# Optimization experiments

Measured on AMD Instinct MI355X. Metric: run time of the kernel, lower is better.

## Reference

```python
import jax, jax.numpy as jnp
import numpy as np

B, S, D = 8, 1024, 768
H, DQK, DV = 12, 64, 64
DHEAD = 2 * DQK + DV  # 192, interleaved per-head qkv layout
DOUT = 768


def setup_inputs() -> dict:
    key = jax.random.key(0)
    k1, k2, k3, k4 = jax.random.split(key, 4)
    x = jax.random.normal(k1, (B, S, D), dtype=jnp.float32)
    w_qkv = jax.random.normal(k2, (D, H * DHEAD), dtype=jnp.float32) * (D ** -0.5)
    w_out = jax.random.normal(k3, (H * DV, DOUT), dtype=jnp.float32) * ((H * DV) ** -0.5)
    b_out = jax.random.normal(k4, (DOUT,), dtype=jnp.float32) * 0.02
    return {"x": x, "w_qkv": w_qkv, "w_out": w_out, "b_out": b_out}


def reference(x, w_qkv, w_out, b_out):
    scale = DQK ** -0.5
    # Interleaved per-head layout: [B,S,H,DHEAD] then split into q|k|v blocks.
    qkv = (x @ w_qkv).reshape(B, S, H, DHEAD)
    q = qkv[..., :DQK]                 # [B,S,H,DQK]
    k = qkv[..., DQK:2 * DQK]          # [B,S,H,DQK]
    v = qkv[..., 2 * DQK:]             # [B,S,H,DV]
    scores = jnp.einsum("bshd,bthd->bhst", q, k) * scale  # [B,H,S,S]
    attn = jax.nn.softmax(scores, axis=-1)
    out = jnp.einsum("bhst,bthd->bshd", attn, v)           # [B,S,H,DV]
    out = out.reshape(B, S, H * DV)
    return out @ w_out + b_out
```

## Files before the change

### kernel.cpp

```cpp
#include <hip/hip_runtime.h>
#include <hip/hip_bf16.h>
#include <cstdint>

namespace {

constexpr int kB = 8;
constexpr int kS = 1024;
constexpr int kD = 768;
constexpr int kH = 12;
constexpr int kDH = 192;
constexpr int kNQ = kH * kDH;
constexpr int kNK = kH * 128;
constexpr int kM = kB * kS;
constexpr int kDO = 768;

using f32x4 = __attribute__((ext_vector_type(4))) float;
using s16x8 = __attribute__((ext_vector_type(8))) short;
using u16x8 = __attribute__((ext_vector_type(8))) unsigned short;
using u16x4 = __attribute__((ext_vector_type(4))) unsigned short;

__device__ __forceinline__ unsigned short f2bf(float f) {
  union { float f; uint32_t u; } v; v.f = f;
  uint32_t u = v.u;
  u += 0x7FFFu + ((u >> 16) & 1u);
  return (unsigned short)(u >> 16);
}

__device__ __forceinline__ void load_lds16(const void* g, void* l) {
  __builtin_amdgcn_global_load_lds((__attribute__((address_space(1))) void*)g,
                                   (__attribute__((address_space(3))) void*)l,
                                   16, 0, 0);
}


__global__ __launch_bounds__(256) void cvt_x_kernel(const float* __restrict__ in,
                                                    unsigned short* __restrict__ out) {
  int i = (blockIdx.x * 256 + threadIdx.x) * 8;
  float4 a = *(const float4*)(in + i);
  float4 b = *(const float4*)(in + i + 4);
  u16x8 o;
  o[0] = f2bf(a.x); o[1] = f2bf(a.y); o[2] = f2bf(a.z); o[3] = f2bf(a.w);
  o[4] = f2bf(b.x); o[5] = f2bf(b.y); o[6] = f2bf(b.z); o[7] = f2bf(b.w);
  *(u16x8*)(out + i) = o;
}

__global__ __launch_bounds__(256) void cvt_transpose_kernel(const float* __restrict__ w,
                                                            unsigned short* __restrict__ wt,
                                                            int K, int N) {
  __shared__ float tile[32][33];
  int k0 = blockIdx.x * 32, n0 = blockIdx.y * 32;
  int tx = threadIdx.x & 31, ty = threadIdx.x >> 5;
  #pragma unroll
  for (int r = 0; r < 32; r += 8)
    tile[ty + r][tx] = w[(size_t)(k0 + ty + r) * N + n0 + tx];
  __syncthreads();
  #pragma unroll
  for (int r = 0; r < 32; r += 8)
    wt[(size_t)(n0 + ty + r) * K + k0 + tx] = f2bf(tile[tx][ty + r]);
}

template <int MODE>
__global__ __launch_bounds__(256, 2) void gemm_bt_kernel(
    const unsigned short* __restrict__ A,
    const unsigned short* __restrict__ Bt,
    void* __restrict__ Cout,
    unsigned short* __restrict__ Vtg,
    const float* __restrict__ bias,
    int M, int N, int K) {
  __shared__ alignas(16) unsigned short Al[128 * 64];
  __shared__ alignas(16) unsigned short Bl[128 * 64];
  const int nT = N >> 7;
  const int tm = blockIdx.x / nT, tn = blockIdx.x % nT;
  const int tid = threadIdx.x;
  const int w = tid >> 6, l = tid & 63;
  const int wr = w >> 1, wc = w & 1;
  const int la = l & 15, g = l >> 4;
  const int sr = l >> 3, sc = l & 7;

  f32x4 acc[4][4] = {};
  const unsigned short* Ag = A + (size_t)(tm * 128) * K;
  const unsigned short* Bg = Bt + (size_t)(tn * 128) * K;

  for (int k0 = 0; k0 < K; k0 += 64) {
    #pragma unroll
    for (int j = 0; j < 4; ++j) {
      int row = w * 32 + j * 8 + sr;
      load_lds16(Ag + (size_t)row * K + k0 + sc * 8, &Al[row * 64 + sc * 8]);
      load_lds16(Bg + (size_t)row * K + k0 + sc * 8, &Bl[row * 64 + sc * 8]);
    }
    __syncthreads();
    #pragma unroll
    for (int kk = 0; kk < 2; ++kk) {
      s16x8 af[4], bfv[4];
      #pragma unroll
      for (int i = 0; i < 4; ++i)
        af[i] = *(const s16x8*)&Al[(wr * 64 + i * 16 + la) * 64 + kk * 32 + g * 8];
      #pragma unroll
      for (int j = 0; j < 4; ++j)
        bfv[j] = *(const s16x8*)&Bl[(wc * 64 + j * 16 + la) * 64 + kk * 32 + g * 8];
      #pragma unroll
      for (int i = 0; i < 4; ++i)
        #pragma unroll
        for (int j = 0; j < 4; ++j)
          acc[i][j] = __builtin_amdgcn_mfma_f32_16x16x32_bf16(af[i], bfv[j], acc[i][j], 0, 0, 0);
    }
    __syncthreads();
  }

  #pragma unroll
  for (int i = 0; i < 4; ++i) {
    int row0 = tm * 128 + wr * 64 + i * 16 + g * 4;
    #pragma unroll
    for (int j = 0; j < 4; ++j) {
      int col = tn * 128 + wc * 64 + j * 16 + la;
      if (MODE == 0) {
        int h = col / kDH, colm = col % kDH;
        if (colm < 128) {
          unsigned short* C = (unsigned short*)Cout;
          float sc2 = (colm < 64) ? 0.125f : 1.0f;
          int ncol = h * 128 + colm;
          #pragma unroll
          for (int r = 0; r < 4; ++r)
            C[(size_t)(row0 + r) * kNK + ncol] = f2bf(acc[i][j][r] * sc2);
        } else {
          int d = colm - 128;
          int bb = row0 >> 10, t = row0 & 1023;
          u16x4 pv;
          #pragma unroll
          for (int r = 0; r < 4; ++r) pv[r] = f2bf(acc[i][j][r]);
          *(u16x4*)&Vtg[((size_t)(bb * kH + h) * 64 + d) * kS + t] = pv;
        }
      } else {
        float* C = (float*)Cout;
        float bv = bias[col];
        #pragma unroll
        for (int r = 0; r < 4; ++r)
          C[(size_t)(row0 + r) * N + col] = acc[i][j][r] + bv;
      }
    }
  }
}

__global__ __launch_bounds__(256, 8) void attn_kernel(
    const unsigned short* __restrict__ qk,
    const unsigned short* __restrict__ Vtg,
    unsigned short* __restrict__ Ab) {
  const int qb = blockIdx.x, h = blockIdx.y, b = blockIdx.z;
  const int tid = threadIdx.x;
  const int w = tid >> 6, l = tid & 63;
  const int la = l & 15, g = l >> 4;

  __shared__ alignas(16) unsigned short Kl[64 * 64];
  __shared__ alignas(16) unsigned short Vl[64 * 64];
  __shared__ alignas(16) unsigned short Pl[64 * 64];

  const size_t base_bs = (size_t)b * kS;
  const size_t qrow0 = base_bs + (size_t)qb * 64;

  s16x8 qf[2];
  {
    const unsigned short* qp = qk + (qrow0 + w * 16 + la) * kNK + h * 128;
    qf[0] = *(const s16x8*)(qp + g * 8);
    qf[1] = *(const s16x8*)(qp + 32 + g * 8);
  }

  const int c0 = w * 64 + l;
  const int c1 = 256 + w * 64 + l;
  const int r0 = c0 >> 3, cc0 = (c0 & 7) ^ (r0 & 7);
  const int r1 = c1 >> 3, cc1 = (c1 & 7) ^ (r1 & 7);
  const unsigned short* Kg = qk + (base_bs)*kNK + h * 128 + 64;
  const unsigned short* Vg = Vtg + (size_t)(b * kH + h) * 64 * kS;

  float mrow[4], lrow[4];
  #pragma unroll
  for (int r = 0; r < 4; ++r) { mrow[r] = -1e30f; lrow[r] = 0.f; }
  f32x4 oacc[4] = {};
  const float LOG2E = 1.44269504088896340736f;

  for (int kt = 0; kt < 16; ++kt) {
    __syncthreads();
    load_lds16(Kg + (size_t)(kt * 64 + r0) * kNK + cc0 * 8, &Kl[c0 * 8]);
    load_lds16(Kg + (size_t)(kt * 64 + r1) * kNK + cc1 * 8, &Kl[c1 * 8]);
    load_lds16(Vg + (size_t)r0 * kS + kt * 64 + cc0 * 8, &Vl[c0 * 8]);
    load_lds16(Vg + (size_t)r1 * kS + kt * 64 + cc1 * 8, &Vl[c1 * 8]);
    __syncthreads();

    f32x4 sacc[4] = {};
    #pragma unroll
    for (int ks = 0; ks < 2; ++ks) {
      #pragma unroll
      for (int tb = 0; tb < 4; ++tb) {
        int row = tb * 16 + la;
        s16x8 kf = *(const s16x8*)&Kl[row * 64 + (((ks * 4 + g) ^ (row & 7)) * 8)];
        sacc[tb] = __builtin_amdgcn_mfma_f32_16x16x32_bf16(qf[ks], kf, sacc[tb], 0, 0, 0);
      }
    }

    #pragma unroll
    for (int r = 0; r < 4; ++r) {
      float m = fmaxf(fmaxf(sacc[0][r], sacc[1][r]), fmaxf(sacc[2][r], sacc[3][r]));
      #pragma unroll
      for (int msk = 1; msk < 16; msk <<= 1) m = fmaxf(m, __shfl_xor(m, msk, 64));
      float mnew = fmaxf(mrow[r], m);
      float corr = exp2f((mrow[r] - mnew) * LOG2E);
      mrow[r] = mnew;
      float s = 0.f;
      #pragma unroll
      for (int tb = 0; tb < 4; ++tb) {
        float p = exp2f((sacc[tb][r] - mnew) * LOG2E);
        sacc[tb][r] = p;
        s += p;
      }
      #pragma unroll
      for (int msk = 1; msk < 16; msk <<= 1) s += __shfl_xor(s, msk, 64);
      lrow[r] = lrow[r] * corr + s;
      #pragma unroll
      for (int db = 0; db < 4; ++db) oacc[db][r] *= corr;
    }

    #pragma unroll
    for (int r = 0; r < 4; ++r) {
      int prow = w * 16 + g * 4 + r, x = prow & 7;
      #pragma unroll
      for (int tb = 0; tb < 4; ++tb) {
        int col = tb * 16 + la;
        Pl[prow * 64 + (col ^ (x << 3))] = f2bf(sacc[tb][r]);
      }
    }

    #pragma unroll
    for (int ks = 0; ks < 2; ++ks) {
      int prow = w * 16 + la;
      s16x8 pf = *(const s16x8*)&Pl[prow * 64 + (((ks * 4 + g) ^ (prow & 7)) * 8)];
      #pragma unroll
      for (int db = 0; db < 4; ++db) {
        int drow = db * 16 + la;
        s16x8 vf = *(const s16x8*)&Vl[drow * 64 + (((ks * 4 + g) ^ (drow & 7)) * 8)];
        oacc[db] = __builtin_amdgcn_mfma_f32_16x16x32_bf16(pf, vf, oacc[db], 0, 0, 0);
      }
    }
  }

  #pragma unroll
  for (int db = 0; db < 4; ++db) {
    #pragma unroll
    for (int r = 0; r < 4; ++r) {
      int row = w * 16 + g * 4 + r;
      Ab[(qrow0 + row) * (size_t)(kH * 64) + h * 64 + db * 16 + la] =
          f2bf(oacc[db][r] / lrow[r]);
    }
  }
}

}

extern "C" void kernel_launch(void* const* d_in, const int* in_sizes, int n_in,
                              void* d_out, int out_size, void* d_ws, size_t ws_size,
                              hipStream_t stream) {
  (void)in_sizes; (void)n_in; (void)out_size; (void)ws_size;
  const float* x = (const float*)d_in[0];
  const float* w_qkv = (const float*)d_in[1];
  const float* w_out = (const float*)d_in[2];
  const float* b_out = (const float*)d_in[3];

  unsigned short* Xb = (unsigned short*)d_ws;
  unsigned short* WqT = Xb + (size_t)kM * kD;
  unsigned short* WoT = WqT + (size_t)kNQ * kD;
  unsigned short* QK = WoT + (size_t)kDO * kDO;
  unsigned short* Vtg = QK + (size_t)kM * kNK;
  unsigned short* Ab = Vtg + (size_t)kB * kH * 64 * kS;

  cvt_x_kernel<<<dim3((kM * kD) / (256 * 8)), dim3(256), 0, stream>>>(x, Xb);
  cvt_transpose_kernel<<<dim3(kD / 32, kNQ / 32), dim3(256), 0, stream>>>(w_qkv, WqT, kD, kNQ);
  cvt_transpose_kernel<<<dim3(kDO / 32, kDO / 32), dim3(256), 0, stream>>>(w_out, WoT, kDO, kDO);

  gemm_bt_kernel<0><<<dim3((kM / 128) * (kNQ / 128)), dim3(256), 0, stream>>>(
      Xb, WqT, (void*)QK, Vtg, nullptr, kM, kNQ, kD);

  attn_kernel<<<dim3(kS / 64, kH, kB), dim3(256), 0, stream>>>(QK, Vtg, Ab);

  gemm_bt_kernel<1><<<dim3((kM / 128) * (kDO / 128)), dim3(256), 0, stream>>>(
      Ab, WoT, d_out, nullptr, b_out, kM, kDO, kH * 64);
}
```

Before: 252.5 us.

## Rewrite attention with 32x32 MFMA, register-resident P and lazy rescaling

```diff
diff --git a/kernel.cpp b/kernel.cpp
--- a/kernel.cpp
+++ b/kernel.cpp
@@ -15,6 +15,7 @@
 constexpr int kDO = 768;
 
 using f32x4 = __attribute__((ext_vector_type(4))) float;
+using f32x16 = __attribute__((ext_vector_type(16))) float;
 using s16x8 = __attribute__((ext_vector_type(8))) short;
 using u16x8 = __attribute__((ext_vector_type(8))) unsigned short;
 using u16x4 = __attribute__((ext_vector_type(4))) unsigned short;
@@ -26,10 +27,32 @@
   return (unsigned short)(u >> 16);
 }
 
+__device__ __forceinline__ unsigned packbf(float a, float b) {
+  return (unsigned)f2bf(a) | ((unsigned)f2bf(b) << 16);
+}
+
 __device__ __forceinline__ void load_lds16(const void* g, void* l) {
   __builtin_amdgcn_global_load_lds((__attribute__((address_space(1))) void*)g,
                                    (__attribute__((address_space(3))) void*)l,
                                    16, 0, 0);
+}
+
+__device__ __forceinline__ s16x8 repack8(int hi, float p0, float p1, float p2, float p3,
+                                         float p4, float p5, float p6, float p7) {
+  unsigned x0 = packbf(p0, p1);
+  unsigned x1 = packbf(p2, p3);
+  unsigned x2 = packbf(p4, p5);
+  unsigned x3 = packbf(p6, p7);
+  unsigned y0 = (unsigned)__shfl_xor((int)x0, 32, 64);
+  unsigned y1 = (unsigned)__shfl_xor((int)x1, 32, 64);
+  unsigned y2 = (unsigned)__shfl_xor((int)x2, 32, 64);
+  unsigned y3 = (unsigned)__shfl_xor((int)x3, 32, 64);
+  union { unsigned u[4]; s16x8 v; } r;
+  r.u[0] = hi ? y2 : x0;
+  r.u[1] = hi ? y3 : x1;
+  r.u[2] = hi ? x2 : y0;
+  r.u[3] = hi ? x3 : y1;
+  return r.v;
 }
 
 
@@ -121,7 +144,9 @@
           int ncol = h * 128 + colm;
           #pragma unroll
           for (int r = 0; r < 4; ++r)
-            C[(size_t)(row0 + r) * kNK + ncol] = f2bf(acc[i][j][r] * sc2);
+            C[(size_t)(row0 + r) * kNK + ncol] = f2bf(acc[i][j][r]
+
+ * sc2);
         } else {
           int d = colm - 128;
           int bb = row0 >> 10, t = row0 & 1023;
@@ -141,41 +166,43 @@
   }
 }
 
-__global__ __launch_bounds__(256, 8) void attn_kernel(
+__global__ __launch_bounds__(256, 3) void attn_kernel(
     const unsigned short* __restrict__ qk,
     const unsigned short* __restrict__ Vtg,
     unsigned short* __restrict__ Ab) {
-  const int qb = blockIdx.x, h = blockIdx.y, b = blockIdx.z;
+  const int id = blockIdx.x;
+  const int b = id & 7;
+  const int h = (id >> 3) % kH;
+  const int qb = id / (kH * 8);
   const int tid = threadIdx.x;
   const int w = tid >> 6, l = tid & 63;
-  const int la = l & 15, g = l >> 4;
+  const int q0 = l & 31, hi = l >> 5;
 
   __shared__ alignas(16) unsigned short Kl[64 * 64];
   __shared__ alignas(16) unsigned short Vl[64 * 64];
-  __shared__ alignas(16) unsigned short Pl[64 * 64];
 
   const size_t base_bs = (size_t)b * kS;
-  const size_t qrow0 = base_bs + (size_t)qb * 64;
-
-  s16x8 qf[2];
+  const size_t qrow0 = base_bs + (size_t)qb * 128;
+  const size_t myq = qrow0 + w * 32 + q0;
+
+  s16x8 qf[4];
   {
-    const unsigned short* qp = qk + (qrow0 + w * 16 + la) * kNK + h * 128;
-    qf[0] = *(const s16x8*)(qp + g * 8);
-    qf[1] = *(const s16x8*)(qp + 32 + g * 8);
+    const unsigned short* qp = qk + myq * kNK + h * 128 + hi * 8;
+    #pragma unroll
+    for (int kg = 0; kg < 4; ++kg) qf[kg] = *(const s16x8*)(qp + kg * 16);
   }
 
   const int c0 = w * 64 + l;
   const int c1 = 256 + w * 64 + l;
   const int r0 = c0 >> 3, cc0 = (c0 & 7) ^ (r0 & 7);
   const int r1 = c1 >> 3, cc1 = (c1 & 7) ^ (r1 & 7);
-  const unsigned short* Kg = qk + (base_bs)*kNK + h * 128 + 64;
+  const unsigned short* Kg = qk + base_bs * kNK + h * 128 + 64;
   const unsigned short* Vg = Vtg + (size_t)(b * kH + h) * 64 * kS;
 
-  float mrow[4], lrow[4];
-  #pragma unroll
-  for (int r = 0; r < 4; ++r) { mrow[r] = -1e30f; lrow[r] = 0.f; }
-  f32x4 oacc[4] = {};
   const float LOG2E = 1.44269504088896340736f;
+  float m2 = -1e30f;
+  float lrow = 0.f;
+  f32x16 oacc[2] = {};
 
   for (int kt = 0; kt < 16; ++kt) {
     __syncthreads();
@@ -185,71 +212,83 @@
     load_lds16(Vg + (size_t)r1 * kS + kt * 64 + cc1 * 8, &Vl[c1 * 8]);
     __syncthreads();
 
-    f32x4 sacc[4] = {};
-    #pragma unroll
-    for (int ks = 0; ks < 2; ++ks) {
-      #pragma unroll
-      for (int tb = 0; tb < 4; ++tb) {
-        int row = tb * 16 + la;
-        s16x8 kf = *(const s16x8*)&Kl[row * 64 + (((ks * 4 + g) ^ (row & 7)) * 8)];
-        sacc[tb] = __builtin_amdgcn_mfma_f32_16x16x32_bf16(qf[ks], kf, sacc[tb], 0, 0, 0);
+    f32x16 sacc[2] = {};
+    #pragma unroll
+    for (int tb = 0; tb < 2; ++tb) {
+      const int tl = tb * 32 + q0, xr = tl & 7;
+      #pragma unroll
+      for (int kg = 0; kg < 4; ++kg) {
+        s16x8 kf = *(const s16x8*)&Kl[tl * 64 + (((kg * 2 + hi) ^ xr) * 8)];
+        sacc[tb] = __builtin_amdgcn_mfma_f32_32x32x16_bf16(kf, qf[kg], sacc[tb], 0, 0, 0);
       }
     }
 
-    #pragma unroll
-    for (int r = 0; r < 4; ++r) {
-      float m = fmaxf(fmaxf(sacc[0][r], sacc[1][r]), fmaxf(sacc[2][r], sacc[3][r]));
-      #pragma unroll
-      for (int msk = 1; msk < 16; msk <<= 1) m = fmaxf(m, __shfl_xor(m, msk, 64));
-      float mnew = fmaxf(mrow[r], m);
-      float corr = exp2f((mrow[r] - mnew) * LOG2E);
-      mrow[r] = mnew;
-      float s = 0.f;
-      #pragma unroll
-      for (int tb = 0; tb < 4; ++tb) {
-        float p = exp2f((sacc[tb][r] - mnew) * LOG2E);
-        sacc[tb][r] = p;
-        s += p;
-      }
-      #pragma unroll
-      for (int msk = 1; msk < 16; msk <<= 1) s += __shfl_xor(s, msk, 64);
-      lrow[r] = lrow[r] * corr + s;
-      #pragma unroll
-      for (int db = 0; db < 4; ++db) oacc[db][r] *= corr;
-    }
-
-    #pragma unroll
-    for (int r = 0; r < 4; ++r) {
-      int prow = w * 16 + g * 4 + r, x = prow & 7;
-      #pragma unroll
-      for (int tb = 0; tb < 4; ++tb) {
-        int col = tb * 16 + la;
-        Pl[prow * 64 + (col ^ (x << 3))] = f2bf(sacc[tb][r]);
-      }
-    }
-
-    #pragma unroll
-    for (int ks = 0; ks < 2; ++ks) {
-      int prow = w * 16 + la;
-      s16x8 pf = *(const s16x8*)&Pl[prow * 64 + (((ks * 4 + g) ^ (prow & 7)) * 8)];
-      #pragma unroll
-      for (int db = 0; db < 4; ++db) {
-        int drow = db * 16 + la;
-        s16x8 vf = *(const s16x8*)&Vl[drow * 64 + (((ks * 4 + g) ^ (drow & 7)) * 8)];
-        oacc[db] = __builtin_amdgcn_mfma_f32_16x16x32_bf16(pf, vf, oacc[db], 0, 0, 0);
-      }
+    float mx[16];
+    #pragma unroll
+    for (int r = 0; r < 16; ++r) mx[r] = fmaxf(sacc[0][r], sacc[1][r]);
+    #pragma unroll
+    for (int s2 = 8; s2 >= 1; s2 >>= 1)
+      #pragma unroll
+      for (int r = 0; r < s2; ++r) mx[r] = fmaxf(mx[r], mx[r + s2]);
+    float pmax = fmaxf(mx[0], __shfl_xor(mx[0], 32, 64));
+    float rx2 = pmax * LOG2E;
+    if (!__all(rx2 - m2 <= 11.5416f)) {
+      float m2n = fmaxf(m2, rx2);
+      float corr = exp2f(m2 - m2n);
+      m2 = m2n;
+      lrow *= corr;
+      #pragma unroll
+      for (int db = 0; db < 2; ++db)
+        #pragma unroll
+        for (int r = 0; r < 16; ++r) oacc[db][r] *= corr;
+    }
+
+    float p[32];
+    #pragma unroll
+    for (int tb = 0; tb < 2; ++tb)
+      #pragma unroll
+      for (int r = 0; r < 16; ++r)
+        p[tb * 16 + r] = exp2f(fmaf(sacc[tb][r], LOG2E, -m2));
+
+    float sm[16];
+    #pragma unroll
+    for (int r = 0; r < 16; ++r) sm[r] = p[r] + p[16 + r];
+    #pragma unroll
+    for (int s2 = 8; s2 >= 1; s2 >>= 1)
+      #pragma unroll
+      for (int r = 0; r < s2; ++r) sm[r] += sm[r + s2];
+    lrow += sm[0] + __shfl_xor(sm[0], 32, 64);
+
+    s16x8 pb0 = repack8(hi, p[0], p[1], p[2], p[3], p[4], p[5], p[6], p[7]);
+    s16x8 pb1 = repack8(hi, p[8], p[9], p[10], p[11], p[12], p[13], p[14], p[15]);
+    s16x8 pb2 = repack8(hi, p[16], p[17], p[18], p[19], p[20], p[21], p[22], p[23]);
+    s16x8 pb3 = repack8(hi, p[24], p[25], p[26], p[27], p[28], p[29], p[30], p[31]);
+
+    #pragma unroll
+    for (int db = 0; db < 2; ++db) {
+      const int dl = db * 32 + q0, xr = dl & 7;
+      s16x8 v0 = *(const s16x8*)&Vl[dl * 64 + (((0 + hi) ^ xr) * 8)];
+      s16x8 v1 = *(const s16x8*)&Vl[dl * 64 + (((2 + hi) ^ xr) * 8)];
+      s16x8 v2 = *(const s16x8*)&Vl[dl * 64 + (((4 + hi) ^ xr) * 8)];
+      s16x8 v3 = *(const s16x8*)&Vl[dl * 64 + (((6 + hi) ^ xr) * 8)];
+      oacc[db] = __builtin_amdgcn_mfma_f32_32x32x16_bf16(v0, pb0, oacc[db], 0, 0, 0);
+      oacc[db] = __builtin_amdgcn_mfma_f32_32x32x16_bf16(v1, pb1, oacc[db], 0, 0, 0);
+      oacc[db] = __builtin_amdgcn_mfma_f32_32x32x16_bf16(v2, pb2, oacc[db], 0, 0, 0);
+      oacc[db] = __builtin_amdgcn_mfma_f32_32x32x16_bf16(v3, pb3, oacc[db], 0, 0, 0);
     }
   }
 
+  float inv = 1.0f / lrow;
+  unsigned short* dst = Ab + myq * (size_t)(kH * 64) + h * 64;
   #pragma unroll
-  for (int db = 0; db < 4; ++db) {
-    #pragma unroll
-    for (int r = 0; r < 4; ++r) {
-      int row = w * 16 + g * 4 + r;
-      Ab[(qrow0 + row) * (size_t)(kH * 64) + h * 64 + db * 16 + la] =
-          f2bf(oacc[db][r] / lrow[r]);
-    }
-  }
+  for (int db = 0; db < 2; ++db)
+    #pragma unroll
+    for (int rq = 0; rq < 4; ++rq) {
+      u16x4 pv;
+      #pragma unroll
+      for (int j = 0; j < 4; ++j) pv[j] = f2bf(oacc[db][rq * 4 + j] * inv);
+      *(u16x4*)&dst[db * 32 + rq * 8 + hi * 4] = pv;
+    }
 }
 
 }
@@ -277,7 +316,7 @@
   gemm_bt_kernel<0><<<dim3((kM / 128) * (kNQ / 128)), dim3(256), 0, stream>>>(
       Xb, WqT, (void*)QK, Vtg, nullptr, kM, kNQ, kD);
 
-  attn_kernel<<<dim3(kS / 64, kH, kB), dim3(256), 0, stream>>>(QK, Vtg, Ab);
+  attn_kernel<<<dim3((kS / 128) * kH * kB), dim3(256), 0, stream>>>(QK, Vtg, Ab);
 
   gemm_bt_kernel<1><<<dim3((kM / 128) * (kDO / 128)), dim3(256), 0, stream>>>(
       Ab, WoT, d_out, nullptr, b_out, kM, kDO, kH * 64);
```

After: 211.0 us. 16.4% less time.
